# Kernel optimization log

Measured on AMD Instinct MI355X. Metric: run time of the kernel, lower is better.

The kernel has to match this reference:

```python
import jax, jax.numpy as jnp
import numpy as np

CDECAY = 0.5      # NEURON_CDECAY = 1/2
VDECAY = 0.75     # NEURON_VDECAY = 3/4
VTH_INIT = 0.5
T = 50            # batch_window
sg = jax.lax.stop_gradient


@jax.custom_vjp
def pseudo_spike(v, vth):
    return (v > vth).astype(v.dtype)

def _ps_fwd(v, vth):
    return pseudo_spike(v, vth), (v, vth)

def _ps_bwd(res, g):
    v, vth = res
    # PseudoSpikeRect: rectangular surrogate gradient, window 0.5; no grad to vth
    return (g * (jnp.abs(v - vth) < 0.5).astype(g.dtype), jnp.zeros_like(vth))

pseudo_spike.defvjp(_ps_fwd, _ps_bwd)


def lif_step(x_in, W, b, u, v_prev, s_prev, temporal):
    """One neuron_model_* call + the temporal-threshold update that follows it."""
    u = u * CDECAY + x_in @ W.T + b
    v = v_prev * VDECAY * (1.0 - s_prev) + u
    # energy threshold term uses detached volts in the original (numpy round-trip)
    energy = jnp.exp((sg(v_prev) - sg(v)) / 3.0) - 1.0
    vth = 0.5 * temporal + 0.5 * energy
    s = pseudo_spike(v, vth)
    vsg = sg(v)  # threshold chain never reaches the loss (custom fn has no vth grad)
    V_m = vsg.mean() - 0.2 * (vsg.max() - vsg.min())
    V_theta = vth.mean() - 0.2 * (vth.max() - vth.min())
    temporal_new = 0.01 * (vsg - V_m) + V_theta + jnp.log(1.0 + jnp.exp((vsg - V_m) / 4.0))
    return u, v, s, temporal_new


def _forward(x, fc1_u, fc1_v, fc1_s, fc2_u, fc2_v, fc2_s, fc3_u, fc3_v, fc3_s,
             fc4_u, fc4_v, fc4_s, W1, b1, W2, b2, W3, b3, W4, b4):
    B = x.shape[0]
    H = W1.shape[0]
    A = W4.shape[0]
    t1 = jnp.full((B, H), VTH_INIT, x.dtype)
    t2 = jnp.full((B, H), VTH_INIT, x.dtype)
    t3 = jnp.full((B, H), VTH_INIT, x.dtype)
    t4 = jnp.full((B, A), VTH_INIT, x.dtype)
    acc = jnp.zeros((B, A), x.dtype)
    xs = jnp.transpose(x, (2, 0, 1))  # [T, B, state_num]

    def step(carry, xt):
        (u1, v1, s1, tt1, u2, v2, s2, tt2, u3, v3, s3, tt3, u4, v4, s4, tt4, a) = carry
        u1, v1, s1, tt1 = lif_step(xt, W1, b1, u1, v1, s1, tt1)
        u2, v2, s2, tt2 = lif_step(s1, W2, b2, u2, v2, s2, tt2)
        u3, v3, s3, tt3 = lif_step(s2, W3, b3, u3, v3, s3, tt3)
        u4, v4, s4, tt4 = lif_step(s3, W4, b4, u4, v4, s4, tt4)
        a = a + s4
        return (u1, v1, s1, tt1, u2, v2, s2, tt2, u3, v3, s3, tt3, u4, v4, s4, tt4, a), None

    carry0 = (fc1_u, fc1_v, fc1_s, t1, fc2_u, fc2_v, fc2_s, t2,
              fc3_u, fc3_v, fc3_s, t3, fc4_u, fc4_v, fc4_s, t4, acc)
    carry, _ = jax.lax.scan(step, carry0, xs)
    return carry[-1] / T  # fc4_sumspike / batch_window


def setup_inputs() -> dict:
    key = jax.random.key(0)
    ks = jax.random.split(key, 10)
    B, S, H, A = 2048, 256, 256, 2
    inp = {"x": jax.random.normal(ks[0], (B, S, T), jnp.float32)}
    for name, shp in [("fc1_u", (B, H)), ("fc1_v", (B, H)), ("fc1_s", (B, H)),
                      ("fc2_u", (B, H)), ("fc2_v", (B, H)), ("fc2_s", (B, H)),
                      ("fc3_u", (B, H)), ("fc3_v", (B, H)), ("fc3_s", (B, H)),
                      ("fc4_u", (B, A)), ("fc4_v", (B, A)), ("fc4_s", (B, A))]:
        inp[name] = jnp.zeros(shp, jnp.float32)
    def lin(k, fan_out, fan_in):
        bound = 1.0 / np.sqrt(fan_in)
        kw, kb = jax.random.split(k)
        W = jax.random.uniform(kw, (fan_out, fan_in), jnp.float32, -bound, bound)
        b = jax.random.uniform(kb, (fan_out,), jnp.float32, -bound, bound)
        return W, b
    inp["W1"], inp["b1"] = lin(ks[1], H, S)
    inp["W2"], inp["b2"] = lin(ks[2], H, H)
    inp["W3"], inp["b3"] = lin(ks[3], H, H)
    inp["W4"], inp["b4"] = lin(ks[4], A, H)
    inp["batch_size"] = B
    return inp


def reference(x, fc1_u, fc1_v, fc1_s, fc2_u, fc2_v, fc2_s, fc3_u, fc3_v, fc3_s,
              fc4_u, fc4_v, fc4_s, W1, b1, W2, b2, W3, b3, W4, b4, batch_size):
    return _forward(x, fc1_u, fc1_v, fc1_s, fc2_u, fc2_v, fc2_s,
                    fc3_u, fc3_v, fc3_s, fc4_u, fc4_v, fc4_s,
                    W1, b1, W2, b2, W3, b3, W4, b4)
```

## Files before the change

### kernel.cpp

```cpp
#include <hip/hip_runtime.h>
#include <cstdint>
#include <cstddef>

#define BB 2048
#define SS 256
#define HH 256
#define AA 2
#define TT 50
#define ROWS  32
#define NTHR  512
#define NLG   64
#define NGRID 192
#define K4PAD 1088
#define WLAYER (64 * K4PAD)
#define LSTR  36
#define S3P   258

struct Params {
  const float* x;
  const float* fu[3]; const float* fv[3]; const float* fs[3];
  const float* f4u; const float* f4v; const float* f4s;
  const float* W[3]; const float* bs[3];
  const float* W4; const float* b4;
  float* out;
  float* wt3;
  float* partials;
  unsigned* flags;
  float* sbuf;
  float* xT;
  int use_xt;
};

__device__ __forceinline__ void pstore(float* p, float v) {
  __hip_atomic_store(p, v, __ATOMIC_RELAXED, __HIP_MEMORY_SCOPE_AGENT);
}
__device__ __forceinline__ float pload(const float* p) {
  return __hip_atomic_load(p, __ATOMIC_RELAXED, __HIP_MEMORY_SCOPE_AGENT);
}
__device__ __forceinline__ unsigned uload_acq(const unsigned* p) {
  return __hip_atomic_load(p, __ATOMIC_ACQUIRE, __HIP_MEMORY_SCOPE_AGENT);
}
__device__ __forceinline__ void ustore_rel(unsigned* p, unsigned v) {
  __hip_atomic_store(p, v, __ATOMIC_RELEASE, __HIP_MEMORY_SCOPE_AGENT);
}
__device__ __forceinline__ void uadd(unsigned* p) {
  __hip_atomic_fetch_add(p, 1u, __ATOMIC_ACQ_REL, __HIP_MEMORY_SCOPE_AGENT);
}

__global__ __launch_bounds__(NTHR, 2)
void snn_pipe(Params p) {
#pragma clang fp contract(off)
  const int tid = threadIdx.x;
  const int blk = blockIdx.x;
  const int L   = blk >> 6;
  const int g   = blk & 63;
  const int B0  = g * ROWS;

  const int h0  = tid & 63;
  const int jg  = tid >> 6;
  const int j0  = jg << 2;
  const int sid = tid & 255;
  const int jq  = tid >> 8;

  __shared__ __align__(16) float in_lds[HH * LSTR];
  __shared__ __align__(16) float s3_lds[ROWS * S3P];
  __shared__ float wred[8][6];
  __shared__ float scal[2][2];
  __shared__ float l4u[64], l4v[64], l4s[64], l4t[64],
                   l4acc[64], l4vn[64], l4vth[64];

  {
    const int gtid = blk * NTHR + tid;
    if (gtid < 16384) {
      const int h = gtid & 255, k4 = gtid >> 8;
      const int hh = h >> 6, hl = h & 63;
      #pragma unroll
      for (int l = 0; l < 3; ++l) {
        float4 w = *reinterpret_cast<const float4*>(p.W[l] + (size_t)h * 256 + k4 * 4);
        *reinterpret_cast<float4*>(
            p.wt3 + (size_t)l * WLAYER + (size_t)k4 * K4PAD + hh * 256 + hl * 4) = w;
      }
    }
    if (p.use_xt) {
      for (int sid0 = gtid; sid0 < BB * SS; sid0 += NGRID * NTHR) {
        const float* src = p.x + (size_t)sid0 * TT;
        #pragma unroll 1
        for (int t = 0; t < TT; ++t)
          p.xT[(size_t)t * (BB * SS) + sid0] = src[t];
      }
    }
  }

  float u[4][4], v[4][4], tp[4][4];
  unsigned smask = 0;
  #pragma unroll
  for (int hh = 0; hh < 4; ++hh)
    #pragma unroll
    for (int jj = 0; jj < 4; ++jj) {
      size_t idx = (size_t)(B0 + j0 + jj) * HH + h0 + 64 * hh;
      u[hh][jj] = p.fu[L][idx];
      v[hh][jj] = p.fv[L][idx];
      if (p.fs[L][idx] != 0.0f) smask |= 1u << (hh * 4 + jj);
      tp[hh][jj] = 0.5f;
    }
  float bL[4];
  #pragma unroll
  for (int hh = 0; hh < 4; ++hh) bL[hh] = p.bs[L][h0 + 64 * hh];
  if (L == 2 && tid < 64) {
    size_t idx = (size_t)(B0 + (tid >> 1)) * AA + (tid & 1);
    l4u[tid] = p.f4u[idx]; l4v[tid] = p.f4v[idx]; l4s[tid] = p.f4s[idx];
    l4t[tid] = 0.5f; l4acc[tid] = 0.0f;
  }
  __syncthreads();

  if (tid == 0) {
    uadd(&p.flags[260]);
    while (uload_acq(&p.flags[260]) < (unsigned)NGRID) __builtin_amdgcn_s_sleep(2);
  }
  __syncthreads();

  const float* wbase = p.wt3 + (size_t)L * WLAYER + (h0 << 2);
  float* sb_in  = (L > 0) ? p.sbuf + (size_t)(L - 1) * 2 * BB * HH : nullptr;
  float* sb_out = (L < 2) ? p.sbuf + (size_t)L * 2 * BB * HH : nullptr;

  #pragma unroll 1
  for (int t = 0; t < TT; ++t) {
    if (L == 0) {
      if (p.use_xt) {
        const float* base = p.xT + (size_t)t * (BB * SS) + (size_t)B0 * SS;
        #pragma unroll
        for (int iq = 0; iq < 4; ++iq) {
          const int j = jq * 16 + iq * 4;
          float4 vv = make_float4(base[(size_t)(j + 0) * SS + sid],
                                  base[(size_t)(j + 1) * SS + sid],
                                  base[(size_t)(j + 2) * SS + sid],
                                  base[(size_t)(j + 3) * SS + sid]);
          *reinterpret_cast<float4*>(&in_lds[sid * LSTR + j]) = vv;
        }
      } else {
        #pragma unroll
        for (int iq = 0; iq < 4; ++iq) {
          const int j = jq * 16 + iq * 4;
          float4 vv = make_float4(
              p.x[((size_t)(B0 + j + 0) * SS + sid) * TT + t],
              p.x[((size_t)(B0 + j + 1) * SS + sid) * TT + t],
              p.x[((size_t)(B0 + j + 2) * SS + sid) * TT + t],
              p.x[((size_t)(B0 + j + 3) * SS + sid) * TT + t]);
          *reinterpret_cast<float4*>(&in_lds[sid * LSTR + j]) = vv;
        }
      }
    } else {
      const int hop = L - 1;
      if (tid == 0) {
        while (uload_acq(&p.flags[hop * 64 + g]) < (unsigned)(t + 1))
          __builtin_amdgcn_s_sleep(2);
      }
      __syncthreads();
      const float* src = sb_in + (size_t)(t & 1) * BB * HH;
      #pragma unroll
      for (int iq = 0; iq < 4; ++iq) {
        const int j = jq * 16 + iq * 4;
        float4 vv = make_float4(pload(src + (size_t)(B0 + j + 0) * HH + sid),
                                pload(src + (size_t)(B0 + j + 1) * HH + sid),
                                pload(src + (size_t)(B0 + j + 2) * HH + sid),
                                pload(src + (size_t)(B0 + j + 3) * HH + sid));
        *reinterpret_cast<float4*>(&in_lds[sid * LSTR + j]) = vv;
      }
      __syncthreads();
      if (tid == 0) ustore_rel(&p.flags[128 + hop * 64 + g], (unsigned)(t + 1));
    }
    __syncthreads();

    float acc[4][4];
    #pragma unroll
    for (int hh = 0; hh < 4; ++hh)
      #pragma unroll
      for (int jj = 0; jj < 4; ++jj) acc[hh][jj] = 0.0f;
    #pragma unroll 2
    for (int k4 = 0; k4 < 64; ++k4) {
      const float* wt = wbase + (size_t)k4 * K4PAD;
      float4 wreg[4];
      #pragma unroll
      for (int hh = 0; hh < 4; ++hh)
        wreg[hh] = *reinterpret_cast<const float4*>(wt + hh * 256);
      #pragma unroll
      for (int q = 0; q < 4; ++q) {
        const int k = k4 * 4 + q;
        float4 iv = *reinterpret_cast<const float4*>(&in_lds[k * LSTR + j0]);
        #pragma unroll
        for (int hh = 0; hh < 4; ++hh) {
          const float w = (q == 0) ? wreg[hh].x : (q == 1) ? wreg[hh].y
                        : (q == 2) ? wreg[hh].z : wreg[hh].w;
          acc[hh][0] = fmaf(iv.x, w, acc[hh][0]);
          acc[hh][1] = fmaf(iv.y, w, acc[hh][1]);
          acc[hh][2] = fmaf(iv.z, w, acc[hh][2]);
          acc[hh][3] = fmaf(iv.w, w, acc[hh][3]);
        }
      }
    }

    if (t > 0) {
      if (tid == 0) {
        while (uload_acq(&p.flags[256 + L]) < (unsigned)(NLG * t))
          __builtin_amdgcn_s_sleep(2);
      }
      __syncthreads();
      {
        const int wv = tid >> 6, ln = tid & 63;
        if (wv == 0 || (wv == 1 && L == 2)) {
          const int ch = (wv == 0) ? L : 3;
          const float* pb = p.partials + (size_t)(ch * 2 + ((t - 1) & 1)) * 6 * 64;
          float r[6];
          #pragma unroll
          for (int st = 0; st < 6; ++st) {
            float rr = pload(pb + st * 64 + ln);
            if (st == 0 || st == 3) {
              #pragma unroll
              for (int m = 1; m < 64; m <<= 1) rr += __shfl_xor(rr, m);
            } else if (st == 1 || st == 4) {
              #pragma unroll
              for (int m = 1; m < 64; m <<= 1) rr = fmaxf(rr, __shfl_xor(rr, m));
            } else {
              #pragma unroll
              for (int m = 1; m < 64; m <<= 1) rr = fminf(rr, __shfl_xor(rr, m));
            }
            r[st] = rr;
          }
          if (ln == 0) {
            const float invN = (ch == 3) ? (1.0f / 4096.0f) : (1.0f / 524288.0f);
            scal[wv][0] = (r[0] * invN) - 0.2f * (r[1] - r[2]);
            scal[wv][1] = (r[3] * invN) - 0.2f * (r[4] - r[5]);
          }
        }
      }
      __syncthreads();
      {
        const float Vm = scal[0][0], Vt = scal[0][1];
        #pragma unroll
        for (int hh = 0; hh < 4; ++hh)
          #pragma unroll
          for (int jj = 0; jj < 4; ++jj) {
            float d = v[hh][jj] - Vm;
            float sp = logf(1.0f + expf(d * 0.25f));
            tp[hh][jj] = (0.01f * d + Vt) + sp;
          }
      }
      if (L == 2 && tid < 64) {
        const float Vm = scal[1][0], Vt = scal[1][1];
        float d = l4v[tid] - Vm;
        float sp = logf(1.0f + expf(d * 0.25f));
        l4t[tid] = (0.01f * d + Vt) + sp;
      }
      __syncthreads();
    }

    float sv = 0.f, svt = 0.f;
    float mxv = -3.402823466e38f, mnv = 3.402823466e38f;
    float mxvt = -3.402823466e38f, mnvt = 3.402823466e38f;
    unsigned nsmask = 0;
    #pragma unroll
    for (int hh = 0; hh < 4; ++hh) {
      const float bbx = bL[hh];
      #pragma unroll
      for (int jj = 0; jj < 4; ++jj) {
        float un = fmaf(u[hh][jj], 0.5f, acc[hh][jj]) + bbx;
        float vp = v[hh][jj];
        float vd = ((smask >> (hh * 4 + jj)) & 1u) ? 0.0f : vp * 0.75f;
        float vn = vd + un;
        float en = expf((vp - vn) / 3.0f) - 1.0f;
        float vt = 0.5f * tp[hh][jj] + 0.5f * en;
        const bool sx = vn > vt;
        u[hh][jj] = un; v[hh][jj] = vn;
        if (sx) nsmask |= 1u << (hh * 4 + jj);
        sv += vn; svt += vt;
        mxv = fmaxf(mxv, vn); mnv = fminf(mnv, vn);
        mxvt = fmaxf(mxvt, vt); mnvt = fminf(mnvt, vt);
      }
    }
    smask = nsmask;
    #pragma unroll
    for (int m = 1; m < 64; m <<= 1) {
      sv += __shfl_xor(sv, m);   svt += __shfl_xor(svt, m);
      mxv = fmaxf(mxv, __shfl_xor(mxv, m));  mnv = fminf(mnv, __shfl_xor(mnv, m));
      mxvt = fmaxf(mxvt, __shfl_xor(mxvt, m)); mnvt = fminf(mnvt, __shfl_xor(mnvt, m));
    }
    if ((tid & 63) == 0) {
      int wv = tid >> 6;
      wred[wv][0] = sv;  wred[wv][1] = mxv;  wred[wv][2] = mnv;
      wred[wv][3] = svt; wred[wv][4] = mxvt; wred[wv][5] = mnvt;
    }
    __syncthreads();

    if (L < 2) {
      if (tid < 6) {
        const int st = tid;
        float r = wred[0][st];
        if (st == 0 || st == 3) {
          #pragma unroll
          for (int wv = 1; wv < 8; ++wv) r = r + wred[wv][st];
        } else if (st == 1 || st == 4) {
          #pragma unroll
          for (int wv = 1; wv < 8; ++wv) r = fmaxf(r, wred[wv][st]);
        } else {
          #pragma unroll
          for (int wv = 1; wv < 8; ++wv) r = fminf(r, wred[wv][st]);
        }
        pstore(p.partials + (size_t)(L * 2 + (t & 1)) * 6 * 64 + st * 64 + g, r);
      }
      if (t >= 2 && tid == 1) {
        while (uload_acq(&p.flags[128 + L * 64 + g]) < (unsigned)(t - 1))
          __builtin_amdgcn_s_sleep(2);
      }
      __syncthreads();
      if (tid == 0) uadd(&p.flags[256 + L]);
      float* dst = sb_out + (size_t)(t & 1) * BB * HH;
      #pragma unroll
      for (int hh = 0; hh < 4; ++hh)
        #pragma unroll
        for (int jj = 0; jj < 4; ++jj)
          pstore(dst + (size_t)(B0 + j0 + jj) * HH + h0 + 64 * hh,
                 ((nsmask >> (hh * 4 + jj)) & 1u) ? 1.0f : 0.0f);
      __syncthreads();
      if (tid == 0) ustore_rel(&p.flags[L * 64 + g], (unsigned)(t + 1));
    } else {
      if (tid < 6) {
        const int st = tid;
        float r = wred[0][st];
        if (st == 0 || st == 3) {
          #pragma unroll
          for (int wv = 1; wv < 8; ++wv) r = r + wred[wv][st];
        } else if (st == 1 || st == 4) {
          #pragma unroll
          for (int wv = 1; wv < 8; ++wv) r = fmaxf(r, wred[wv][st]);
        } else {
          #pragma unroll
          for (int wv = 1; wv < 8; ++wv) r = fminf(r, wred[wv][st]);
        }
        pstore(p.partials + (size_t)(2 * 2 + (t & 1)) * 6 * 64 + st * 64 + g, r);
      }
      #pragma unroll
      for (int hh = 0; hh < 4; ++hh)
        #pragma unroll
        for (int jj = 0; jj < 4; ++jj)
          s3_lds[(j0 + jj) * S3P + h0 + 64 * hh] =
              ((nsmask >> (hh * 4 + jj)) & 1u) ? 1.0f : 0.0f;
      __syncthreads();

      {
        const int d = tid >> 3, c = tid & 7;
        if (d < 64) {
          const int j4 = d >> 1, a4 = d & 1;
          float part = 0.0f;
          #pragma unroll
          for (int i = 0; i < 32; ++i) {
            int k = c + 8 * i;
            part = fmaf(s3_lds[j4 * S3P + k], p.W4[a4 * HH + k], part);
          }
          #pragma unroll
          for (int m = 1; m < 8; m <<= 1) part += __shfl_xor(part, m);
          if (c == 0) {
            float un = fmaf(l4u[d], 0.5f, part) + p.b4[a4];
            float vp = l4v[d];
            float vd = (vp * 0.75f) * (1.0f - l4s[d]);
            float vn = vd + un;
            float en = expf((vp - vn) / 3.0f) - 1.0f;
            float vt = 0.5f * l4t[d] + 0.5f * en;
            float sx = (vn > vt) ? 1.0f : 0.0f;
            l4u[d] = un; l4v[d] = vn; l4s[d] = sx;
            l4acc[d] += sx; l4vn[d] = vn; l4vth[d] = vt;
          }
        }
      }
      __syncthreads();

      if (tid < 64) {
        float a = l4vn[tid], b = l4vth[tid];
        float s4 = a, mx4 = a, mn4 = a;
        float st4 = b, mxt4 = b, mnt4 = b;
        #pragma unroll
        for (int m = 1; m < 64; m <<= 1) {
          s4  += __shfl_xor(s4, m);   st4 += __shfl_xor(st4, m);
          mx4  = fmaxf(mx4,  __shfl_xor(mx4, m));  mn4  = fminf(mn4,  __shfl_xor(mn4, m));
          mxt4 = fmaxf(mxt4, __shfl_xor(mxt4, m)); mnt4 = fminf(mnt4, __shfl_xor(mnt4, m));
        }
        if (tid == 0) {
          float* pp = p.partials + (size_t)(3 * 2 + (t & 1)) * 6 * 64 + g;
          pstore(pp + 0 * 64, s4);   pstore(pp + 1 * 64, mx4);  pstore(pp + 2 * 64, mn4);
          pstore(pp + 3 * 64, st4);  pstore(pp + 4 * 64, mxt4); pstore(pp + 5 * 64, mnt4);
        }
      }
      __syncthreads();
      if (tid == 0) uadd(&p.flags[256 + L]);
    }
  }

  if (L == 2 && tid < 64)
    p.out[(size_t)(B0 + (tid >> 1)) * AA + (tid & 1)] = l4acc[tid] / 50.0f;
}

extern "C" void kernel_launch(void* const* d_in, const int* in_sizes, int n_in,
                              void* d_out, int out_size, void* d_ws, size_t ws_size,
                              hipStream_t stream) {
  Params p;
  p.x     = (const float*)d_in[0];
  p.fu[0] = (const float*)d_in[1];  p.fv[0] = (const float*)d_in[2];  p.fs[0] = (const float*)d_in[3];
  p.fu[1] = (const float*)d_in[4];  p.fv[1] = (const float*)d_in[5];  p.fs[1] = (const float*)d_in[6];
  p.fu[2] = (const float*)d_in[7];  p.fv[2] = (const float*)d_in[8];  p.fs[2] = (const float*)d_in[9];
  p.f4u   = (const float*)d_in[10]; p.f4v   = (const float*)d_in[11]; p.f4s   = (const float*)d_in[12];
  p.W[0]  = (const float*)d_in[13]; p.bs[0] = (const float*)d_in[14];
  p.W[1]  = (const float*)d_in[15]; p.bs[1] = (const float*)d_in[16];
  p.W[2]  = (const float*)d_in[17]; p.bs[2] = (const float*)d_in[18];
  p.W4    = (const float*)d_in[19]; p.b4    = (const float*)d_in[20];
  p.out   = (float*)d_out;

  float* ws   = (float*)d_ws;
  p.wt3       = ws;
  p.partials  = ws + 208896;
  p.flags     = (unsigned*)(ws + 211968);
  p.sbuf      = ws + 212992;
  p.xT        = ws + 2310144;
  size_t need = ((size_t)2310144 + (size_t)TT * BB * SS) * sizeof(float);
  p.use_xt    = (ws_size >= need) ? 1 : 0;

  hipMemsetAsync((void*)p.flags, 0, 4096, stream);
  snn_pipe<<<dim3(NGRID), dim3(NTHR), 0, stream>>>(p);
}
```

Baseline: 1.826 ms.

## Remap matmul thread tile to 4x4 outer product over contiguous neurons

Changes the thread-to-output mapping so each thread owns 4 contiguous hidden neurons by 4 batch rows, with waves split into hidden quarters and batch halves. The transposed weight layout becomes k-major with row stride 272, so each k step loads one float4 of weights per k and one float4 of inputs, feeding a 16-FMA outer product. State loads, bias loads and spike stores become contiguous float4/row accesses. The aim is fewer weight loads per FMA and better coalescing. The cost is a new LDS input access pattern with possible bank conflicts and a different padded layout.

```diff
diff --git a/kernel.cpp b/kernel.cpp
--- a/kernel.cpp
+++ b/kernel.cpp
@@ -11,8 +11,8 @@
 #define NTHR  512
 #define NLG   64
 #define NGRID 192
-#define K4PAD 1088
-#define WLAYER (64 * K4PAD)
+#define KSTR  272
+#define WLAYER (256 * KSTR)
 #define LSTR  36
 #define S3P   258
 
@@ -47,6 +47,24 @@
   __hip_atomic_fetch_add(p, 1u, __ATOMIC_ACQ_REL, __HIP_MEMORY_SCOPE_AGENT);
 }
 
+#define OUTER(IV, WV)                                        \
+  acc[0][0] = fmaf((IV).x, (WV).x, acc[0][0]);               \
+  acc[0][1] = fmaf((IV).x, (WV).y, acc[0][1]);               \
+  acc[0][2] = fmaf((IV).x, (WV).z, acc[0][2]);               \
+  acc[0][3] = fmaf((IV).x, (WV).w, acc[0][3]);               \
+  acc[1][0] = fmaf((IV).y, (WV).x, acc[1][0]);               \
+  acc[1][1] = fmaf((IV).y, (WV).y, acc[1][1]);               \
+  acc[1][2] = fmaf((IV).y, (WV).z, acc[1][2]);               \
+  acc[1][3] = fmaf((IV).y, (WV).w, acc[1][3]);               \
+  acc[2][0] = fmaf((IV).z, (WV).x, acc[2][0]);               \
+  acc[2][1] = fmaf((IV).z, (WV).y, acc[2][1]);               \
+  acc[2][2] = fmaf((IV).z, (WV).z, acc[2][2]);               \
+  acc[2][3] = fmaf((IV).z, (WV).w, acc[2][3]);               \
+  acc[3][0] = fmaf((IV).w, (WV).x, acc[3][0]);               \
+  acc[3][1] = fmaf((IV).w, (WV).y, acc[3][1]);               \
+  acc[3][2] = fmaf((IV).w, (WV).z, acc[3][2]);               \
+  acc[3][3] = fmaf((IV).w, (WV).w, acc[3][3]);
+
 __global__ __launch_bounds__(NTHR, 2)
 void snn_pipe(Params p) {
 #pragma clang fp contract(off)
@@ -56,9 +74,15 @@
   const int g   = blk & 63;
   const int B0  = g * ROWS;
 
-  const int h0  = tid & 63;
-  const int jg  = tid >> 6;
-  const int j0  = jg << 2;
+  const int w    = tid >> 6;
+  const int l    = tid & 63;
+  const int hp   = w & 3;
+  const int qp   = w >> 2;
+  const int hsel = l & 15;
+  const int jsel = l >> 4;
+  const int hb   = hp * 64 + hsel * 4;
+  const int jb   = qp * 16 + jsel * 4;
+
   const int sid = tid & 255;
   const int jq  = tid >> 8;
 
@@ -72,13 +96,13 @@
   {
     const int gtid = blk * NTHR + tid;
     if (gtid < 16384) {
-      const int h = gtid & 255, k4 = gtid >> 8;
-      const int hh = h >> 6, hl = h & 63;
-      #pragma unroll
-      for (int l = 0; l < 3; ++l) {
-        float4 w = *reinterpret_cast<const float4*>(p.W[l] + (size_t)h * 256 + k4 * 4);
-        *reinterpret_cast<float4*>(
-            p.wt3 + (size_t)l * WLAYER + (size_t)k4 * K4PAD + hh * 256 + hl * 4) = w;
+      const int h = gtid & 255, kq = gtid >> 8;
+      #pragma unroll
+      for (int ll = 0; ll < 3; ++ll) {
+        float4 wv = *reinterpret_cast<const float4*>(p.W[ll] + (size_t)h * 256 + kq * 4);
+        float* dst = p.wt3 + (size_t)ll * WLAYER + (size_t)(kq * 4) * KSTR + h;
+        dst[0 * KSTR] = wv.x; dst[1 * KSTR] = wv.y;
+        dst[2 * KSTR] = wv.z; dst[3 * KSTR] = wv.w;
       }
     }
     if (p.use_xt) {
@@ -94,18 +118,22 @@
   float u[4][4], v[4][4], tp[4][4];
   unsigned smask = 0;
   #pragma unroll
-  for (int hh = 0; hh < 4; ++hh)
+  for (int jj = 0; jj < 4; ++jj) {
+    size_t idx = (size_t)(B0 + jb + jj) * HH + hb;
+    float4 uu = *reinterpret_cast<const float4*>(p.fu[L] + idx);
+    float4 vv = *reinterpret_cast<const float4*>(p.fv[L] + idx);
+    float4 ss = *reinterpret_cast<const float4*>(p.fs[L] + idx);
+    u[jj][0] = uu.x; u[jj][1] = uu.y; u[jj][2] = uu.z; u[jj][3] = uu.w;
+    v[jj][0] = vv.x; v[jj][1] = vv.y; v[jj][2] = vv.z; v[jj][3] = vv.w;
+    if (ss.x != 0.0f) smask |= 1u << (jj * 4 + 0);
+    if (ss.y != 0.0f) smask |= 1u << (jj * 4 + 1);
+    if (ss.z != 0.0f) smask |= 1u << (jj * 4 + 2);
+    if (ss.w != 0.0f) smask |= 1u << (jj * 4 + 3);
     #pragma unroll
-    for (int jj = 0; jj < 4; ++jj) {
-      size_t idx = (size_t)(B0 + j0 + jj) * HH + h0 + 64 * hh;
-      u[hh][jj] = p.fu[L][idx];
-      v[hh][jj] = p.fv[L][idx];
-      if (p.fs[L][idx] != 0.0f) smask |= 1u << (hh * 4 + jj);
-      tp[hh][jj] = 0.5f;
-    }
-  float bL[4];
-  #pragma unroll
-  for (int hh = 0; hh < 4; ++hh) bL[hh] = p.bs[L][h0 + 64 * hh];
+    for (int i = 0; i < 4; ++i) tp[jj][i] = 0.5f;
+  }
+  const float4 bb4 = *reinterpret_cast<const float4*>(p.bs[L] + hb);
+  const float bL[4] = { bb4.x, bb4.y, bb4.z, bb4.w };
   if (L == 2 && tid < 64) {
     size_t idx = (size_t)(B0 + (tid >> 1)) * AA + (tid & 1);
     l4u[tid] = p.f4u[idx]; l4v[tid] = p.f4v[idx]; l4s[tid] = p.f4s[idx];
@@ -119,7 +147,7 @@
   }
   __syncthreads();
 
-  const float* wbase = p.wt3 + (size_t)L * WLAYER + (h0 << 2);
+  const float* wbase = p.wt3 + (size_t)L * WLAYER + hb;
   float* sb_in  = (L > 0) ? p.sbuf + (size_t)(L - 1) * 2 * BB * HH : nullptr;
   float* sb_out = (L < 2) ? p.sbuf + (size_t)L * 2 * BB * HH : nullptr;
 
@@ -173,30 +201,25 @@
 
     float acc[4][4];
     #pragma unroll
-    for (int hh = 0; hh < 4; ++hh)
-      #pragma unroll
-      for (int jj = 0; jj < 4; ++jj) acc[hh][jj] = 0.0f;
+    for (int jj = 0; jj < 4; ++jj)
+      #pragma unroll
+      for (int i = 0; i < 4; ++i) acc[jj][i] = 0.0f;
     #pragma unroll 2
     for (int k4 = 0; k4 < 64; ++k4) {
-      const float* wt = wbase + (size_t)k4 * K4PAD;
-      float4 wreg[4];
-      #pragma unroll
-      for (int hh = 0; hh < 4; ++hh)
-        wreg[hh] = *reinterpret_cast<const float4*>(wt + hh * 256);
-      #pragma unroll
-      for (int q = 0; q < 4; ++q) {
-        const int k = k4 * 4 + q;
-        float4 iv = *reinterpret_cast<const float4*>(&in_lds[k * LSTR + j0]);
-        #pragma unroll
-        for (int hh = 0; hh < 4; ++hh) {
-          const float w = (q == 0) ? wreg[hh].x : (q == 1) ? wreg[hh].y
-                        : (q == 2) ? wreg[hh].z : wreg[hh].w;
-          acc[hh][0] = fmaf(iv.x, w, acc[hh][0]);
-          acc[hh][1] = fmaf(iv.y, w, acc[hh][1]);
-          acc[hh][2] = fmaf(iv.z, w, acc[hh][2]);
-          acc[hh][3] = fmaf(iv.w, w, acc[hh][3]);
-        }
-      }
+      const float* wk = wbase + (size_t)(k4 * 4) * KSTR;
+      float4 w0 = *reinterpret_cast<const float4*>(wk);
+      float4 w1 = *reinterpret_cast<const float4*>(wk + KSTR);
+      float4 w2 = *reinterpret_cast<const float4*>(wk + 2 * KSTR);
+      float4 w3 = *reinterpret_cast<const float4*>(wk + 3 * KSTR);
+      const float* ib = &in_lds[(k4 * 4) * LSTR + jb];
+      float4 i0 = *reinterpret_cast<const float4*>(ib);
+      float4 i1 = *reinterpret_cast<const float4*>(ib + LSTR);
+      float4 i2 = *reinterpret_cast<const float4*>(ib + 2 * LSTR);
+      float4 i3 = *reinterpret_cast<const float4*>(ib + 3 * LSTR);
+      OUTER(i0, w0);
+      OUTER(i1, w1);
+      OUTER(i2, w2);
+      OUTER(i3, w3);
     }
 
     if (t > 0) {
@@ -237,12 +260,12 @@
       {
         const float Vm = scal[0][0], Vt = scal[0][1];
         #pragma unroll
-        for (int hh = 0; hh < 4; ++hh)
-          #pragma unroll
-          for (int jj = 0; jj < 4; ++jj) {
-            float d = v[hh][jj] - Vm;
+        for (int jj = 0; jj < 4; ++jj)
+          #pragma unroll
+          for (int i = 0; i < 4; ++i) {
+            float d = v[jj][i] - Vm;
             float sp = logf(1.0f + expf(d * 0.25f));
-            tp[hh][jj] = (0.01f * d + Vt) + sp;
+            tp[jj][i] = (0.01f * d + Vt) + sp;
           }
       }
       if (L == 2 && tid < 64) {
@@ -259,19 +282,18 @@
     float mxvt = -3.402823466e38f, mnvt = 3.402823466e38f;
     unsigned nsmask = 0;
     #pragma unroll
-    for (int hh = 0; hh < 4; ++hh) {
-      const float bbx = bL[hh];
-      #pragma unroll
-      for (int jj = 0; jj < 4; ++jj) {
-        float un = fmaf(u[hh][jj], 0.5f, acc[hh][jj]) + bbx;
-        float vp = v[hh][jj];
-        float vd = ((smask >> (hh * 4 + jj)) & 1u) ? 0.0f : vp * 0.75f;
+    for (int jj = 0; jj < 4; ++jj) {
+      #pragma unroll
+      for (int i = 0; i < 4; ++i) {
+        float un = fmaf(u[jj][i], 0.5f, acc[jj][i]) + bL[i];
+        float vp = v[jj][i];
+        float vd = ((smask >> (jj * 4 + i)) & 1u) ? 0.0f : vp * 0.75f;
         float vn = vd + un;
         float en = expf((vp - vn) / 3.0f) - 1.0f;
-        float vt = 0.5f * tp[hh][jj] + 0.5f * en;
+        float vt = 0.5f * tp[jj][i] + 0.5f * en;
         const bool sx = vn > vt;
-        u[hh][jj] = un; v[hh][jj] = vn;
-        if (sx) nsmask |= 1u << (hh * 4 + jj);
+        u[jj][i] = un; v[jj][i] = vn;
+        if (sx) nsmask |= 1u << (jj * 4 + i);
         sv += vn; svt += vt;
         mxv = fmaxf(mxv, vn); mnv = fminf(mnv, vn);
         mxvt = fmaxf(mxvt, vt); mnvt = fminf(mnvt, vt);
@@ -315,11 +337,12 @@
       if (tid == 0) uadd(&p.flags[256 + L]);
       float* dst = sb_out + (size_t)(t & 1) * BB * HH;
       #pragma unroll
-      for (int hh = 0; hh < 4; ++hh)
-        #pragma unroll
-        for (int jj = 0; jj < 4; ++jj)
-          pstore(dst + (size_t)(B0 + j0 + jj) * HH + h0 + 64 * hh,
-                 ((nsmask >> (hh * 4 + jj)) & 1u) ? 1.0f : 0.0f);
+      for (int jj = 0; jj < 4; ++jj) {
+        float* drow = dst + (size_t)(B0 + jb + jj) * HH + hb;
+        #pragma unroll
+        for (int i = 0; i < 4; ++i)
+          pstore(drow + i, ((nsmask >> (jj * 4 + i)) & 1u) ? 1.0f : 0.0f);
+      }
       __syncthreads();
       if (tid == 0) ustore_rel(&p.flags[L * 64 + g], (unsigned)(t + 1));
     } else {
@@ -339,11 +362,12 @@
         pstore(p.partials + (size_t)(2 * 2 + (t & 1)) * 6 * 64 + st * 64 + g, r);
       }
       #pragma unroll
-      for (int hh = 0; hh < 4; ++hh)
-        #pragma unroll
-        for (int jj = 0; jj < 4; ++jj)
-          s3_lds[(j0 + jj) * S3P + h0 + 64 * hh] =
-              ((nsmask >> (hh * 4 + jj)) & 1u) ? 1.0f : 0.0f;
+      for (int jj = 0; jj < 4; ++jj) {
+        float* srow = &s3_lds[(jb + jj) * S3P + hb];
+        #pragma unroll
+        for (int i = 0; i < 4; ++i)
+          srow[i] = ((nsmask >> (jj * 4 + i)) & 1u) ? 1.0f : 0.0f;
+      }
       __syncthreads();
 
       {
```

New measurement: 1.920 ms. 5.1% more time.
